# Kernel optimization log

Measured on AMD Instinct MI355X. Metric: run time of the kernel, lower is better.

## Reference

```python
import jax, jax.numpy as jnp
import numpy as np

NUM_GRAPHS = 8
NEG_SLOPE = 0.2  # PyG GATConv default negative_slope


def gat_dense(x, W, att_src, att_dst, W_edge, att_edge, bias, agg, mask):
    """Dense-masked equivalent of PyG GATConv(edge_dim=1, add_self_loops=True,
    fill_value='mean'). mask[i,j]=True means edge src=i -> dst=j."""
    N = x.shape[0]
    H, C = att_src.shape
    h = (x @ W).reshape(N, H, C)                      # [N,H,C]
    a_s = jnp.einsum('nhc,hc->nh', h, att_src)        # alpha_src per node
    a_d = jnp.einsum('nhc,hc->nh', h, att_dst)        # alpha_dst per node
    eye = jnp.eye(N, dtype=bool)
    mask_od = mask & ~eye                             # remove_self_loops
    ev = jnp.where(mask_od, agg, 0.0)                 # edge_attr (scalar per edge)
    cnt = mask_od.sum(axis=0)                         # in-degree per dst
    mean_e = jnp.where(cnt > 0, ev.sum(axis=0) / jnp.maximum(cnt, 1), 0.0)
    ev = ev + jnp.eye(N, dtype=agg.dtype) * mean_e    # add self-loops, fill='mean' per dst
    full = mask_od | eye
    # lin_edge is Linear(1, H*C, bias=False): per-head edge score is
    # e_ij * sum_c W_edge[h,c]*att_edge[h,c]
    we = (W_edge.reshape(H, C) * att_edge).sum(-1)    # [H]
    logits = jax.nn.leaky_relu(a_s[:, None, :] + a_d[None, :, :] + ev[:, :, None] * we[None, None, :], NEG_SLOPE)  # [src,dst,H]
    logits = jnp.where(full[:, :, None], logits, -jnp.inf)
    alpha = jax.nn.softmax(logits, axis=0)            # segment softmax over sources per dst
    out = jnp.einsum('sdh,shc->dhc', alpha, h).reshape(N, H * C) + bias
    return out


def setup_inputs() -> dict:
    key = jax.random.key(0)
    ks = jax.random.split(key, 20)
    N, IN, HID, H, OUT = 2048, 128, 64, 4, 10
    s = 0.05
    rn = lambda k, shp, sc=s: (jax.random.normal(k, shp, dtype=jnp.float32) * sc)
    return {
        'x': jax.random.normal(ks[0], (N, IN), dtype=jnp.float32),
        'attn_tensor': jax.random.normal(ks[1], (12, N, N), dtype=jnp.float32),
        'batch_idx': jnp.sort(jax.random.randint(ks[2], (N,), 0, NUM_GRAPHS)),
        # Conv2d(12,1,1) -> 1x1 conv == weighted sum over the 12 maps
        'w_agg': rn(ks[3], (12,), 0.2),
        'b_agg': jnp.zeros((), dtype=jnp.float32),
        # GAT layer 1: in=128 -> heads=4, out=64, concat
        'W1': rn(ks[4], (IN, H * HID)),
        'att_src1': rn(ks[5], (H, HID)),
        'att_dst1': rn(ks[6], (H, HID)),
        'We1': rn(ks[7], (1, H * HID)),
        'att_e1': rn(ks[8], (H, HID)),
        'bias1': jnp.zeros((H * HID,), dtype=jnp.float32),
        # GAT layer 2: in=256 -> heads=1, out=64
        'W2': rn(ks[9], (H * HID, HID)),
        'att_src2': rn(ks[10], (1, HID)),
        'att_dst2': rn(ks[11], (1, HID)),
        'We2': rn(ks[12], (1, HID)),
        'att_e2': rn(ks[13], (1, HID)),
        'bias2': jnp.zeros((HID,), dtype=jnp.float32),
        # final Linear(hidden, out)
        'W_lin': rn(ks[14], (HID, OUT)),
        'b_lin': jnp.zeros((OUT,), dtype=jnp.float32),
    }


def reference(x, attn_tensor, batch_idx, w_agg, b_agg, W1, att_src1, att_dst1,
              We1, att_e1, bias1, W2, att_src2, att_dst2, We2, att_e2, bias2,
              W_lin, b_lin):
    # 1x1 conv over the 12 attention maps -> [N,N]
    agg = jnp.einsum('k,kij->ij', w_agg, attn_tensor) + b_agg
    mask = agg > 0.0  # threshold
    h1 = jax.nn.elu(gat_dense(x, W1, att_src1, att_dst1, We1, att_e1, bias1, agg, mask))
    h2 = jax.nn.elu(gat_dense(h1, W2, att_src2, att_dst2, We2, att_e2, bias2, agg, mask))
    # global mean pool over graphs
    ones = jnp.ones((x.shape[0],), dtype=h2.dtype)
    cnt = jax.ops.segment_sum(ones, batch_idx, num_segments=NUM_GRAPHS)
    g = jax.ops.segment_sum(h2, batch_idx, num_segments=NUM_GRAPHS) / jnp.maximum(cnt, 1.0)[:, None]
    out = g @ W_lin + b_lin
    # edge_attr = agg[mask]; returned densely (masked) to keep static shapes
    edge_attr = jnp.where(mask, agg, 0.0)
    return out, edge_attr
```

## Files before the change

kernel.cpp:

```cpp
#include <hip/hip_runtime.h>

#define N 2048
#define NG 8

__device__ __forceinline__ float lrelu(float x) { return x > 0.f ? x : 0.2f * x; }

__global__ __launch_bounds__(256) void aggK(const float* __restrict__ attn,
                                            const float* __restrict__ w_agg,
                                            const float* __restrict__ b_agg,
                                            float* __restrict__ edge_out,
                                            float* __restrict__ aggT,
                                            float* __restrict__ colSum,
                                            float* __restrict__ colCnt) {
  __shared__ float tile[32][33];
  __shared__ float wsh[12];
  __shared__ float cs[32];
  __shared__ float cc[32];
  int tx = threadIdx.x, ty = threadIdx.y;
  int tid = ty * 32 + tx;
  if (tid < 12) wsh[tid] = w_agg[tid];
  if (tid < 32) { cs[tid] = 0.f; cc[tid] = 0.f; }
  __syncthreads();
  int i0 = blockIdx.y * 32, j0 = blockIdx.x * 32;
  int j = j0 + tx;
  float bb = b_agg[0];
#pragma unroll
  for (int r = 0; r < 4; ++r) {
    int li = ty + 8 * r;
    int i = i0 + li;
    const float* p = attn + (size_t)i * N + j;
    float v = bb;
#pragma unroll
    for (int k = 0; k < 12; ++k) v += wsh[k] * p[(size_t)k * N * N];
    float e = v > 0.f ? v : 0.f;
    edge_out[(size_t)i * N + j] = e;
    tile[li][tx] = e;
    if (e > 0.f && i != j) { atomicAdd(&cs[tx], e); atomicAdd(&cc[tx], 1.f); }
  }
  __syncthreads();
#pragma unroll
  for (int r = 0; r < 4; ++r) {
    int lj = ty + 8 * r;
    aggT[(size_t)(j0 + lj) * N + i0 + tx] = tile[tx][lj];
  }
  if (tid < 32) {
    atomicAdd(&colSum[j0 + tid], cs[tid]);
    atomicAdd(&colCnt[j0 + tid], cc[tid]);
  }
}

__global__ __launch_bounds__(256) void h1K(const float* __restrict__ x, const float* __restrict__ W1,
                                           const float* __restrict__ att_src1, const float* __restrict__ att_dst1,
                                           const float* __restrict__ We1, const float* __restrict__ att_e1,
                                           const float* __restrict__ We2, const float* __restrict__ att_e2,
                                           float* __restrict__ h1, float* __restrict__ a_s1, float* __restrict__ a_d1,
                                           float* __restrict__ we) {
  __shared__ float xr[4][128];
  int tid = threadIdx.x;
  int n0 = blockIdx.x * 4;
  if (blockIdx.x == 0) {
    float v1 = We1[tid] * att_e1[tid];
#pragma unroll
    for (int off = 32; off > 0; off >>= 1) v1 += __shfl_down(v1, off);
    int lane = tid & 63, wid = tid >> 6;
    if (lane == 0) we[wid] = v1;
    float v2 = (tid < 64) ? We2[tid] * att_e2[tid] : 0.f;
#pragma unroll
    for (int off = 32; off > 0; off >>= 1) v2 += __shfl_down(v2, off);
    if (tid == 0) we[4] = v2;
  }
  for (int t = tid; t < 512; t += 256) xr[t >> 7][t & 127] = x[n0 * 128 + t];
  __syncthreads();
  float acc[4] = {0.f, 0.f, 0.f, 0.f};
  for (int k = 0; k < 128; ++k) {
    float wv = W1[k * 256 + tid];
#pragma unroll
    for (int r = 0; r < 4; ++r) acc[r] += xr[r][k] * wv;
  }
  float asw = att_src1[tid], adw = att_dst1[tid];
  int lane = tid & 63, head = tid >> 6;
#pragma unroll
  for (int r = 0; r < 4; ++r) {
    h1[(size_t)(n0 + r) * 256 + tid] = acc[r];
    float ps = acc[r] * asw, pd = acc[r] * adw;
#pragma unroll
    for (int off = 32; off > 0; off >>= 1) { ps += __shfl_down(ps, off); pd += __shfl_down(pd, off); }
    if (lane == 0) { a_s1[(n0 + r) * 4 + head] = ps; a_d1[(n0 + r) * 4 + head] = pd; }
  }
}

__global__ __launch_bounds__(256) void pv1K(const float* __restrict__ aggT, const float* __restrict__ h1,
                                            const float* __restrict__ a_s1, const float* __restrict__ a_d1,
                                            const float* __restrict__ colSum, const float* __restrict__ colCnt,
                                            const float* __restrict__ we,
                                            float* __restrict__ partials, float* __restrict__ z1) {
  __shared__ float hT[16][260];
  __shared__ float pL[16][260];
  int tid = threadIdx.x;
  int d0 = blockIdx.x * 64;
  int sBeg = blockIdx.y * 128;
  float w0 = we[0], w1 = we[1], w2 = we[2], w3 = we[3];
  int ssp = tid & 15, dq = tid >> 4;
  float4 ad4[4];
  float me_[4];
#pragma unroll
  for (int q = 0; q < 4; ++q) {
    int d = d0 + dq * 4 + q;
    ad4[q] = *(const float4*)(a_d1 + d * 4);
    float c = colCnt[d];
    me_[q] = c > 0.f ? colSum[d] / c : 0.f;
  }
  float zac[4][4];
#pragma unroll
  for (int q = 0; q < 4; ++q)
#pragma unroll
    for (int h = 0; h < 4; ++h) zac[q][h] = 0.f;
  int dg = tid & 7;
  int cb = (tid >> 3) * 8;
  int hh = tid >> 6;
  float acc[8][8];
#pragma unroll
  for (int i = 0; i < 8; ++i)
#pragma unroll
    for (int j = 0; j < 8; ++j) acc[i][j] = 0.f;

  int c4 = (tid & 63) * 4;
  int rb = (tid >> 6) * 4;

#pragma unroll 1
  for (int s0 = sBeg; s0 < sBeg + 128; s0 += 16) {
#pragma unroll
    for (int p4 = 0; p4 < 4; ++p4) {
      int r = rb + p4;
      *(float4*)(&hT[r][c4]) = *(const float4*)(h1 + (size_t)(s0 + r) * 256 + c4);
    }
    {
      int s = s0 + ssp;
      float4 as4 = *(const float4*)(a_s1 + s * 4);
      float pq[4][4];
#pragma unroll
      for (int q = 0; q < 4; ++q) {
        int d = d0 + dq * 4 + q;
        float av = aggT[(size_t)d * N + s];
        float ev; bool inc;
        if (s == d) { ev = me_[q]; inc = true; } else { ev = av; inc = av > 0.f; }
        float p0 = inc ? __expf(lrelu(as4.x + ad4[q].x + ev * w0)) : 0.f;
        float p1 = inc ? __expf(lrelu(as4.y + ad4[q].y + ev * w1)) : 0.f;
        float p2 = inc ? __expf(lrelu(as4.z + ad4[q].z + ev * w2)) : 0.f;
        float p3 = inc ? __expf(lrelu(as4.w + ad4[q].w + ev * w3)) : 0.f;
        pq[0][q] = p0; pq[1][q] = p1; pq[2][q] = p2; pq[3][q] = p3;
        zac[q][0] += p0; zac[q][1] += p1; zac[q][2] += p2; zac[q][3] += p3;
      }
#pragma unroll
      for (int h = 0; h < 4; ++h)
        *(float4*)(&pL[ssp][h * 64 + dq * 4]) = make_float4(pq[h][0], pq[h][1], pq[h][2], pq[h][3]);
    }
    __syncthreads();
#pragma unroll
    for (int ss = 0; ss < 16; ++ss) {
      float4 pA = *(const float4*)(&pL[ss][hh * 64 + dg * 8]);
      float4 pB = *(const float4*)(&pL[ss][hh * 64 + dg * 8 + 4]);
      float4 hA = *(const float4*)(&hT[ss][cb]);
      float4 hB = *(const float4*)(&hT[ss][cb + 4]);
      float pv[8] = {pA.x, pA.y, pA.z, pA.w, pB.x, pB.y, pB.z, pB.w};
      float hv[8] = {hA.x, hA.y, hA.z, hA.w, hB.x, hB.y, hB.z, hB.w};
#pragma unroll
      for (int di = 0; di < 8; ++di)
#pragma unroll
        for (int ci = 0; ci < 8; ++ci) acc[di][ci] += pv[di] * hv[ci];
    }
    __syncthreads();
  }
  float* outp = partials + (size_t)blockIdx.y * ((size_t)N * 256);
#pragma unroll
  for (int di = 0; di < 8; ++di) {
    size_t rowo = (size_t)(d0 + dg * 8 + di) * 256 + cb;
    *(float4*)(outp + rowo) = make_float4(acc[di][0], acc[di][1], acc[di][2], acc[di][3]);
    *(float4*)(outp + rowo + 4) = make_float4(acc[di][4], acc[di][5], acc[di][6], acc[di][7]);
  }
#pragma unroll
  for (int q = 0; q < 4; ++q)
#pragma unroll
    for (int h = 0; h < 4; ++h) {
      float v = zac[q][h];
      v += __shfl_down(v, 8); v += __shfl_down(v, 4);
      v += __shfl_down(v, 2); v += __shfl_down(v, 1);
      if (ssp == 0) atomicAdd(&z1[(d0 + dq * 4 + q) * 4 + h], v);
    }
}

__global__ __launch_bounds__(256) void h2K(const float* __restrict__ partials, const float* __restrict__ z1,
                                           const float* __restrict__ bias1,
                                           const float* __restrict__ W2,
                                           const float* __restrict__ att_src2, const float* __restrict__ att_dst2,
                                           float* __restrict__ hh2, float* __restrict__ a_s2, float* __restrict__ a_d2) {
  __shared__ float hr[4][256];
  int tid = threadIdx.x;
  int n0 = blockIdx.x * 4;
  for (int e = tid; e < 1024; e += 256) {
    int node = e >> 8, c = e & 255;
    size_t base = (size_t)(n0 + node) * 256 + c;
    float sAcc = 0.f;
#pragma unroll
    for (int q = 0; q < 16; ++q) sAcc += partials[(size_t)q * N * 256 + base];
    float a = sAcc / z1[(n0 + node) * 4 + (c >> 6)] + bias1[c];
    hr[node][c] = a > 0.f ? a : __expf(a) - 1.f;
  }
  __syncthreads();
  int c = tid & 63, nl = tid >> 6;
  float acc = 0.f;
  for (int k = 0; k < 256; ++k) acc += hr[nl][k] * W2[k * 64 + c];
  hh2[(size_t)(n0 + nl) * 64 + c] = acc;
  float ps = acc * att_src2[c], pd = acc * att_dst2[c];
#pragma unroll
  for (int off = 32; off > 0; off >>= 1) { ps += __shfl_down(ps, off); pd += __shfl_down(pd, off); }
  if (c == 0) { a_s2[n0 + nl] = ps; a_d2[n0 + nl] = pd; }
}

__global__ __launch_bounds__(256) void pv2K(const float* __restrict__ aggT, const float* __restrict__ hh2,
                                            const float* __restrict__ a_s2, const float* __restrict__ a_d2,
                                            const float* __restrict__ colSum, const float* __restrict__ colCnt,
                                            const float* __restrict__ we,
                                            float* __restrict__ partials, float* __restrict__ z2) {
  __shared__ float hT[16][68];
  __shared__ float pL[16][132];
  int tid = threadIdx.x;
  int d0 = blockIdx.x * 128;
  int sBeg = blockIdx.y * 64;
  float wE = we[4];
  int ssp = tid & 15, dq = tid >> 4;
  float adv[8], me_[8];
#pragma unroll
  for (int q = 0; q < 8; ++q) {
    int d = d0 + dq * 8 + q;
    adv[q] = a_d2[d];
    float c = colCnt[d];
    me_[q] = c > 0.f ? colSum[d] / c : 0.f;
  }
  float zac[8];
#pragma unroll
  for (int q = 0; q < 8; ++q) zac[q] = 0.f;
  int dg = tid & 15;
  int cg = tid >> 4;
  float acc[8][4];
#pragma unroll
  for (int i = 0; i < 8; ++i)
#pragma unroll
    for (int j = 0; j < 4; ++j) acc[i][j] = 0.f;

  int stR = tid >> 4, stC = (tid & 15) * 4;

#pragma unroll 1
  for (int s0 = sBeg; s0 < sBeg + 64; s0 += 16) {
    *(float4*)(&hT[stR][stC]) = *(const float4*)(hh2 + (size_t)(s0 + stR) * 64 + stC);
    {
      int s = s0 + ssp;
      float asv = a_s2[s];
      float pq[8];
#pragma unroll
      for (int q = 0; q < 8; ++q) {
        int d = d0 + dq * 8 + q;
        float av = aggT[(size_t)d * N + s];
        float ev; bool inc;
        if (s == d) { ev = me_[q]; inc = true; } else { ev = av; inc = av > 0.f; }
        float p = inc ? __expf(lrelu(asv + adv[q] + ev * wE)) : 0.f;
        pq[q] = p;
        zac[q] += p;
      }
      *(float4*)(&pL[ssp][dq * 8])     = make_float4(pq[0], pq[1], pq[2], pq[3]);
      *(float4*)(&pL[ssp][dq * 8 + 4]) = make_float4(pq[4], pq[5], pq[6], pq[7]);
    }
    __syncthreads();
#pragma unroll
    for (int ss = 0; ss < 16; ++ss) {
      float4 pA = *(const float4*)(&pL[ss][dg * 8]);
      float4 pB = *(const float4*)(&pL[ss][dg * 8 + 4]);
      float4 hA = *(const float4*)(&hT[ss][cg * 4]);
      float pv[8] = {pA.x, pA.y, pA.z, pA.w, pB.x, pB.y, pB.z, pB.w};
      float hv[4] = {hA.x, hA.y, hA.z, hA.w};
#pragma unroll
      for (int di = 0; di < 8; ++di)
#pragma unroll
        for (int ci = 0; ci < 4; ++ci) acc[di][ci] += pv[di] * hv[ci];
    }
    __syncthreads();
  }
  float* outp = partials + (size_t)blockIdx.y * ((size_t)N * 64);
#pragma unroll
  for (int di = 0; di < 8; ++di) {
    size_t rowo = (size_t)(d0 + dg * 8 + di) * 64 + cg * 4;
    *(float4*)(outp + rowo) = make_float4(acc[di][0], acc[di][1], acc[di][2], acc[di][3]);
  }
#pragma unroll
  for (int q = 0; q < 8; ++q) {
    float v = zac[q];
    v += __shfl_down(v, 8); v += __shfl_down(v, 4);
    v += __shfl_down(v, 2); v += __shfl_down(v, 1);
    if (ssp == 0) atomicAdd(&z2[d0 + dq * 8 + q], v);
  }
}

__global__ __launch_bounds__(256) void fin2K(const float* __restrict__ partials, const float* __restrict__ z2,
                                             const float* __restrict__ bias2, float* __restrict__ h2post) {
  int i = blockIdx.x * 256 + threadIdx.x;
  int d = i >> 6, c = i & 63;
  float s = 0.f;
#pragma unroll
  for (int q = 0; q < 32; ++q) s += partials[(size_t)q * N * 64 + i];
  float a = s / z2[d] + bias2[c];
  h2post[i] = a > 0.f ? a : __expf(a) - 1.f;
}

__global__ __launch_bounds__(256) void poolK(const float* __restrict__ h2post, const int* __restrict__ bidx,
                                             const float* __restrict__ W_lin, const float* __restrict__ b_lin,
                                             float* __restrict__ out) {
  __shared__ float red[4][64];
  __shared__ float cntA[4];
  __shared__ float gsh[64];
  int tid = threadIdx.x;
  int b = blockIdx.x;
  int c = tid & 63, g = tid >> 6;
  float s = 0.f, cnt = 0.f;
  for (int n = g; n < N; n += 4) {
    if (bidx[n] == b) {
      s += h2post[(size_t)n * 64 + c];
      cnt += 1.f;
    }
  }
  red[g][c] = s;
  if (c == 0) cntA[g] = cnt;
  __syncthreads();
  if (g == 0) {
    float tot = red[0][c] + red[1][c] + red[2][c] + red[3][c];
    float ct = cntA[0] + cntA[1] + cntA[2] + cntA[3];
    gsh[c] = tot / fmaxf(ct, 1.f);
  }
  __syncthreads();
  if (tid < 10) {
    float o = b_lin[tid];
    for (int k = 0; k < 64; ++k) o += gsh[k] * W_lin[k * 10 + tid];
    out[b * 10 + tid] = o;
  }
}

extern "C" void kernel_launch(void* const* d_in, const int* in_sizes, int n_in,
                              void* d_out, int out_size, void* d_ws, size_t ws_size,
                              hipStream_t stream) {
  const float* x        = (const float*)d_in[0];
  const float* attn     = (const float*)d_in[1];
  const int*   bidx     = (const int*)d_in[2];
  const float* w_agg    = (const float*)d_in[3];
  const float* b_agg    = (const float*)d_in[4];
  const float* W1       = (const float*)d_in[5];
  const float* att_src1 = (const float*)d_in[6];
  const float* att_dst1 = (const float*)d_in[7];
  const float* We1      = (const float*)d_in[8];
  const float* att_e1   = (const float*)d_in[9];
  const float* bias1    = (const float*)d_in[10];
  const float* W2       = (const float*)d_in[11];
  const float* att_src2 = (const float*)d_in[12];
  const float* att_dst2 = (const float*)d_in[13];
  const float* We2      = (const float*)d_in[14];
  const float* att_e2   = (const float*)d_in[15];
  const float* bias2    = (const float*)d_in[16];
  const float* W_lin    = (const float*)d_in[17];
  const float* b_lin    = (const float*)d_in[18];

  float* out = (float*)d_out;
  float* edge_out = out + 80;

  float* w = (float*)d_ws;
  size_t o = 0;
  float* aggT   = w + o; o += (size_t)N * N;
  float* zb     = w + o; o += 7 * N;
  float* wev    = w + o; o += 8;
  float* h1     = w + o; o += (size_t)N * 256;
  float* a_s1   = w + o; o += (size_t)N * 4;
  float* a_d1   = w + o; o += (size_t)N * 4;
  float* hh2    = w + o; o += (size_t)N * 64;
  float* a_s2   = w + o; o += N;
  float* a_d2   = w + o; o += N;
  float* partials = w + o; o += (size_t)16 * N * 256;

  float* colSum = zb;
  float* colCnt = zb + N;
  float* z1     = zb + 2 * N;
  float* z2     = zb + 6 * N;
  float* h2post = hh2;

  hipMemsetAsync(zb, 0, 7 * N * sizeof(float), stream);
  aggK<<<dim3(64, 64), dim3(32, 8), 0, stream>>>(attn, w_agg, b_agg, edge_out, aggT, colSum, colCnt);
  h1K<<<512, 256, 0, stream>>>(x, W1, att_src1, att_dst1, We1, att_e1, We2, att_e2, h1, a_s1, a_d1, wev);
  pv1K<<<dim3(32, 16), 256, 0, stream>>>(aggT, h1, a_s1, a_d1, colSum, colCnt, wev, partials, z1);
  h2K<<<512, 256, 0, stream>>>(partials, z1, bias1, W2, att_src2, att_dst2, hh2, a_s2, a_d2);
  pv2K<<<dim3(16, 32), 256, 0, stream>>>(aggT, hh2, a_s2, a_d2, colSum, colCnt, wev, partials, z2);
  fin2K<<<512, 256, 0, stream>>>(partials, z2, bias2, h2post);
  poolK<<<NG, 256, 0, stream>>>(h2post, bidx, W_lin, b_lin, out);
}
```

Before: 549.6 us.

## Drop transposed agg copy, fuse agg with h1 and fin2 with pooling

The separate transposed aggT matrix is removed. Both attention-value kernels now read the row-major edge_out output directly, using float4 loads along the destination dimension, which avoids writing and re-reading a 16 MB buffer. The aggregation and h1 projection kernels are merged into one launch split by block index, so they can run concurrently. fin2 and pooling are merged using atomics and a last-block ticket that computes the final linear layer. This saves launches and memory traffic, at the cost of global atomics and a nondeterministic summation order in pooling.

```diff
diff --git a/kernel.cpp b/kernel.cpp
--- a/kernel.cpp
+++ b/kernel.cpp
@@ -5,91 +5,85 @@
 
 __device__ __forceinline__ float lrelu(float x) { return x > 0.f ? x : 0.2f * x; }
 
-__global__ __launch_bounds__(256) void aggK(const float* __restrict__ attn,
-                                            const float* __restrict__ w_agg,
-                                            const float* __restrict__ b_agg,
-                                            float* __restrict__ edge_out,
-                                            float* __restrict__ aggT,
-                                            float* __restrict__ colSum,
-                                            float* __restrict__ colCnt) {
-  __shared__ float tile[32][33];
-  __shared__ float wsh[12];
-  __shared__ float cs[32];
-  __shared__ float cc[32];
-  int tx = threadIdx.x, ty = threadIdx.y;
-  int tid = ty * 32 + tx;
-  if (tid < 12) wsh[tid] = w_agg[tid];
-  if (tid < 32) { cs[tid] = 0.f; cc[tid] = 0.f; }
-  __syncthreads();
-  int i0 = blockIdx.y * 32, j0 = blockIdx.x * 32;
-  int j = j0 + tx;
-  float bb = b_agg[0];
-#pragma unroll
-  for (int r = 0; r < 4; ++r) {
-    int li = ty + 8 * r;
-    int i = i0 + li;
-    const float* p = attn + (size_t)i * N + j;
-    float v = bb;
-#pragma unroll
-    for (int k = 0; k < 12; ++k) v += wsh[k] * p[(size_t)k * N * N];
-    float e = v > 0.f ? v : 0.f;
-    edge_out[(size_t)i * N + j] = e;
-    tile[li][tx] = e;
-    if (e > 0.f && i != j) { atomicAdd(&cs[tx], e); atomicAdd(&cc[tx], 1.f); }
-  }
-  __syncthreads();
-#pragma unroll
-  for (int r = 0; r < 4; ++r) {
-    int lj = ty + 8 * r;
-    aggT[(size_t)(j0 + lj) * N + i0 + tx] = tile[tx][lj];
-  }
-  if (tid < 32) {
-    atomicAdd(&colSum[j0 + tid], cs[tid]);
-    atomicAdd(&colCnt[j0 + tid], cc[tid]);
-  }
-}
-
-__global__ __launch_bounds__(256) void h1K(const float* __restrict__ x, const float* __restrict__ W1,
-                                           const float* __restrict__ att_src1, const float* __restrict__ att_dst1,
-                                           const float* __restrict__ We1, const float* __restrict__ att_e1,
-                                           const float* __restrict__ We2, const float* __restrict__ att_e2,
-                                           float* __restrict__ h1, float* __restrict__ a_s1, float* __restrict__ a_d1,
-                                           float* __restrict__ we) {
-  __shared__ float xr[4][128];
-  int tid = threadIdx.x;
-  int n0 = blockIdx.x * 4;
-  if (blockIdx.x == 0) {
-    float v1 = We1[tid] * att_e1[tid];
-#pragma unroll
-    for (int off = 32; off > 0; off >>= 1) v1 += __shfl_down(v1, off);
-    int lane = tid & 63, wid = tid >> 6;
-    if (lane == 0) we[wid] = v1;
-    float v2 = (tid < 64) ? We2[tid] * att_e2[tid] : 0.f;
-#pragma unroll
-    for (int off = 32; off > 0; off >>= 1) v2 += __shfl_down(v2, off);
-    if (tid == 0) we[4] = v2;
-  }
-  for (int t = tid; t < 512; t += 256) xr[t >> 7][t & 127] = x[n0 * 128 + t];
-  __syncthreads();
-  float acc[4] = {0.f, 0.f, 0.f, 0.f};
-  for (int k = 0; k < 128; ++k) {
-    float wv = W1[k * 256 + tid];
-#pragma unroll
-    for (int r = 0; r < 4; ++r) acc[r] += xr[r][k] * wv;
-  }
-  float asw = att_src1[tid], adw = att_dst1[tid];
-  int lane = tid & 63, head = tid >> 6;
-#pragma unroll
-  for (int r = 0; r < 4; ++r) {
-    h1[(size_t)(n0 + r) * 256 + tid] = acc[r];
-    float ps = acc[r] * asw, pd = acc[r] * adw;
-#pragma unroll
-    for (int off = 32; off > 0; off >>= 1) { ps += __shfl_down(ps, off); pd += __shfl_down(pd, off); }
-    if (lane == 0) { a_s1[(n0 + r) * 4 + head] = ps; a_d1[(n0 + r) * 4 + head] = pd; }
-  }
-}
-
-__global__ __launch_bounds__(256) void pv1K(const float* __restrict__ aggT, const float* __restrict__ h1,
+__global__ __launch_bounds__(256) void aggh1K(const float* __restrict__ attn,
+                                              const float* __restrict__ w_agg,
+                                              const float* __restrict__ b_agg,
+                                              const float* __restrict__ x,
+                                              const float* __restrict__ W1,
+                                              const float* __restrict__ att_src1,
+                                              const float* __restrict__ att_dst1,
+                                              const float* __restrict__ We1, const float* __restrict__ att_e1,
+                                              const float* __restrict__ We2, const float* __restrict__ att_e2,
+                                              float* __restrict__ edge_out,
+                                              float* __restrict__ colSum, float* __restrict__ colCnt,
+                                              float* __restrict__ h1, float* __restrict__ a_s1, float* __restrict__ a_d1,
+                                              float* __restrict__ we) {
+  __shared__ float smem[512];
+  int tid = threadIdx.x;
+  if (blockIdx.x < 512) {
+    float* xr = smem;
+    int n0 = blockIdx.x * 4;
+    if (blockIdx.x == 0) {
+      float v1 = We1[tid] * att_e1[tid];
+#pragma unroll
+      for (int off = 32; off > 0; off >>= 1) v1 += __shfl_down(v1, off);
+      int lane = tid & 63, wid = tid >> 6;
+      if (lane == 0) we[wid] = v1;
+      float v2 = (tid < 64) ? We2[tid] * att_e2[tid] : 0.f;
+#pragma unroll
+      for (int off = 32; off > 0; off >>= 1) v2 += __shfl_down(v2, off);
+      if (tid == 0) we[4] = v2;
+    }
+    for (int t = tid; t < 512; t += 256) xr[t] = x[n0 * 128 + t];
+    __syncthreads();
+    float acc[4] = {0.f, 0.f, 0.f, 0.f};
+    for (int k = 0; k < 128; ++k) {
+      float wv = W1[k * 256 + tid];
+#pragma unroll
+      for (int r = 0; r < 4; ++r) acc[r] += xr[r * 128 + k] * wv;
+    }
+    float asw = att_src1[tid], adw = att_dst1[tid];
+    int lane = tid & 63, head = tid >> 6;
+#pragma unroll
+    for (int r = 0; r < 4; ++r) {
+      h1[(size_t)(n0 + r) * 256 + tid] = acc[r];
+      float ps = acc[r] * asw, pd = acc[r] * adw;
+#pragma unroll
+      for (int off = 32; off > 0; off >>= 1) { ps += __shfl_down(ps, off); pd += __shfl_down(pd, off); }
+      if (lane == 0) { a_s1[(n0 + r) * 4 + head] = ps; a_d1[(n0 + r) * 4 + head] = pd; }
+    }
+  } else {
+    float* wsh = smem;
+    float* cs = smem + 32;
+    float* cc = smem + 64;
+    int bidA = blockIdx.x - 512;
+    int tx = tid & 31, ty = tid >> 5;
+    if (tid < 12) wsh[tid] = w_agg[tid];
+    if (tid < 32) { cs[tid] = 0.f; cc[tid] = 0.f; }
+    __syncthreads();
+    int i0 = (bidA >> 6) * 32, j0 = (bidA & 63) * 32;
+    int j = j0 + tx;
+    float bb = b_agg[0];
+#pragma unroll
+    for (int r = 0; r < 4; ++r) {
+      int i = i0 + ty + 8 * r;
+      const float* p = attn + (size_t)i * N + j;
+      float v = bb;
+#pragma unroll
+      for (int k = 0; k < 12; ++k) v += wsh[k] * p[(size_t)k * N * N];
+      float e = v > 0.f ? v : 0.f;
+      edge_out[(size_t)i * N + j] = e;
+      if (e > 0.f && i != j) { atomicAdd(&cs[tx], e); atomicAdd(&cc[tx], 1.f); }
+    }
+    __syncthreads();
+    if (tid < 32) {
+      atomicAdd(&colSum[j0 + tid], cs[tid]);
+      atomicAdd(&colCnt[j0 + tid], cc[tid]);
+    }
+  }
+}
+
+__global__ __launch_bounds__(256) void pv1K(const float* __restrict__ edge, const float* __restrict__ h1,
                                             const float* __restrict__ a_s1, const float* __restrict__ a_d1,
                                             const float* __restrict__ colSum, const float* __restrict__ colCnt,
                                             const float* __restrict__ we,
@@ -137,11 +131,13 @@
     {
       int s = s0 + ssp;
       float4 as4 = *(const float4*)(a_s1 + s * 4);
+      float4 av4 = *(const float4*)(edge + (size_t)s * N + d0 + dq * 4);
+      float ev_[4] = {av4.x, av4.y, av4.z, av4.w};
       float pq[4][4];
 #pragma unroll
       for (int q = 0; q < 4; ++q) {
         int d = d0 + dq * 4 + q;
-        float av = aggT[(size_t)d * N + s];
+        float av = ev_[q];
         float ev; bool inc;
         if (s == d) { ev = me_[q]; inc = true; } else { ev = av; inc = av > 0.f; }
         float p0 = inc ? __expf(lrelu(as4.x + ad4[q].x + ev * w0)) : 0.f;
@@ -217,7 +213,7 @@
   if (c == 0) { a_s2[n0 + nl] = ps; a_d2[n0 + nl] = pd; }
 }
 
-__global__ __launch_bounds__(256) void pv2K(const float* __restrict__ aggT, const float* __restrict__ hh2,
+__global__ __launch_bounds__(256) void pv2K(const float* __restrict__ edge, const float* __restrict__ hh2,
                                             const float* __restrict__ a_s2, const float* __restrict__ a_d2,
                                             const float* __restrict__ colSum, const float* __restrict__ colCnt,
                                             const float* __restrict__ we,
@@ -256,11 +252,14 @@
     {
       int s = s0 + ssp;
       float asv = a_s2[s];
+      float4 eA = *(const float4*)(edge + (size_t)s * N + d0 + dq * 8);
+      float4 eB = *(const float4*)(edge + (size_t)s * N + d0 + dq * 8 + 4);
+      float ev_[8] = {eA.x, eA.y, eA.z, eA.w, eB.x, eB.y, eB.z, eB.w};
       float pq[8];
 #pragma unroll
       for (int q = 0; q < 8; ++q) {
         int d = d0 + dq * 8 + q;
-        float av = aggT[(size_t)d * N + s];
+        float av = ev_[q];
         float ev; bool inc;
         if (s == d) { ev = me_[q]; inc = true; } else { ev = av; inc = av > 0.f; }
         float p = inc ? __expf(lrelu(asv + adv[q] + ev * wE)) : 0.f;
@@ -300,46 +299,46 @@
   }
 }
 
-__global__ __launch_bounds__(256) void fin2K(const float* __restrict__ partials, const float* __restrict__ z2,
-                                             const float* __restrict__ bias2, float* __restrict__ h2post) {
-  int i = blockIdx.x * 256 + threadIdx.x;
+__global__ __launch_bounds__(256) void fin2poolK(const float* __restrict__ partials, const float* __restrict__ z2,
+                                                 const float* __restrict__ bias2, const int* __restrict__ bidx,
+                                                 const float* __restrict__ W_lin, const float* __restrict__ b_lin,
+                                                 float* __restrict__ gsum, float* __restrict__ gcnt,
+                                                 int* __restrict__ ticket, float* __restrict__ out) {
+  int tid = threadIdx.x;
+  int i = blockIdx.x * 256 + tid;
   int d = i >> 6, c = i & 63;
   float s = 0.f;
 #pragma unroll
   for (int q = 0; q < 32; ++q) s += partials[(size_t)q * N * 64 + i];
   float a = s / z2[d] + bias2[c];
-  h2post[i] = a > 0.f ? a : __expf(a) - 1.f;
-}
-
-__global__ __launch_bounds__(256) void poolK(const float* __restrict__ h2post, const int* __restrict__ bidx,
-                                             const float* __restrict__ W_lin, const float* __restrict__ b_lin,
-                                             float* __restrict__ out) {
-  __shared__ float red[4][64];
-  __shared__ float cntA[4];
-  __shared__ float gsh[64];
-  int tid = threadIdx.x;
-  int b = blockIdx.x;
-  int c = tid & 63, g = tid >> 6;
-  float s = 0.f, cnt = 0.f;
-  for (int n = g; n < N; n += 4) {
-    if (bidx[n] == b) {
-      s += h2post[(size_t)n * 64 + c];
-      cnt += 1.f;
-    }
-  }
-  red[g][c] = s;
-  if (c == 0) cntA[g] = cnt;
+  float v = a > 0.f ? a : __expf(a) - 1.f;
+  int g = bidx[d];
+  atomicAdd(&gsum[g * 64 + c], v);
+  if (c == 0) atomicAdd(&gcnt[g], 1.f);
+  __threadfence();
   __syncthreads();
-  if (g == 0) {
-    float tot = red[0][c] + red[1][c] + red[2][c] + red[3][c];
-    float ct = cntA[0] + cntA[1] + cntA[2] + cntA[3];
-    gsh[c] = tot / fmaxf(ct, 1.f);
+  __shared__ int lastSh;
+  if (tid == 0) {
+    int t = atomicAdd(ticket, 1);
+    lastSh = (t == (int)gridDim.x - 1) ? 1 : 0;
   }
   __syncthreads();
-  if (tid < 10) {
-    float o = b_lin[tid];
-    for (int k = 0; k < 64; ++k) o += gsh[k] * W_lin[k * 10 + tid];
-    out[b * 10 + tid] = o;
+  if (lastSh) {
+    __shared__ float gm[NG][64];
+    __shared__ float cnt_[NG];
+    if (tid < NG) cnt_[tid] = atomicAdd(&gcnt[tid], 0.f);
+    __syncthreads();
+    for (int e = tid; e < NG * 64; e += 256) {
+      float sv = atomicAdd(&gsum[e], 0.f);
+      gm[e >> 6][e & 63] = sv / fmaxf(cnt_[e >> 6], 1.f);
+    }
+    __syncthreads();
+    if (tid < NG * 10) {
+      int b = tid / 10, o = tid % 10;
+      float accv = b_lin[o];
+      for (int k = 0; k < 64; ++k) accv += gm[b][k] * W_lin[k * 10 + o];
+      out[b * 10 + o] = accv;
+    }
   }
 }
 
@@ -371,29 +370,30 @@
 
   float* w = (float*)d_ws;
   size_t o = 0;
-  float* aggT   = w + o; o += (size_t)N * N;
-  float* zb     = w + o; o += 7 * N;
-  float* wev    = w + o; o += 8;
-  float* h1     = w + o; o += (size_t)N * 256;
-  float* a_s1   = w + o; o += (size_t)N * 4;
-  float* a_d1   = w + o; o += (size_t)N * 4;
-  float* hh2    = w + o; o += (size_t)N * 64;
-  float* a_s2   = w + o; o += N;
-  float* a_d2   = w + o; o += N;
+  float* zb   = w + o; o += 7 * N + 1024;
+  float* wev  = w + o; o += 8;
+  float* h1   = w + o; o += (size_t)N * 256;
+  float* a_s1 = w + o; o += (size_t)N * 4;
+  float* a_d1 = w + o; o += (size_t)N * 4;
+  float* hh2  = w + o; o += (size_t)N * 64;
+  float* a_s2 = w + o; o += N;
+  float* a_d2 = w + o; o += N;
   float* partials = w + o; o += (size_t)16 * N * 256;
 
   float* colSum = zb;
   float* colCnt = zb + N;
   float* z1     = zb + 2 * N;
   float* z2     = zb + 6 * N;
-  float* h2post = hh2;
-
-  hipMemsetAsync(zb, 0, 7 * N * sizeof(float), stream);
-  aggK<<<dim3(64, 64), dim3(32, 8), 0, stream>>>(attn, w_agg, b_agg, edge_out, aggT, colSum, colCnt);
-  h1K<<<512, 256, 0, stream>>>(x, W1, att_src1, att_dst1, We1, att_e1, We2, att_e2, h1, a_s1, a_d1, wev);
-  pv1K<<<dim3(32, 16), 256, 0, stream>>>(aggT, h1, a_s1, a_d1, colSum, colCnt, wev, partials, z1);
+  float* gsum   = zb + 7 * N;
+  float* gcnt   = zb + 7 * N + 512;
+  int*   ticket = (int*)(zb + 7 * N + 520);
+
+  hipMemsetAsync(zb, 0, (7 * N + 1024) * sizeof(float), stream);
+  aggh1K<<<4608, 256, 0, stream>>>(attn, w_agg, b_agg, x, W1, att_src1, att_dst1,
+                                   We1, att_e1, We2, att_e2,
+                                   edge_out, colSum, colCnt, h1, a_s1, a_d1, wev);
+  pv1K<<<dim3(32, 16), 256, 0, stream>>>(edge_out, h1, a_s1, a_d1, colSum, colCnt, wev, partials, z1);
   h2K<<<512, 256, 0, stream>>>(partials, z1, bias1, W2, att_src2, att_dst2, hh2, a_s2, a_d2);
-  pv2K<<<dim3(16, 32), 256, 0, stream>>>(aggT, hh2, a_s2, a_d2, colSum, colCnt, wev, partials, z2);
-  fin2K<<<512, 256, 0, stream>>>(partials, z2, bias2, h2post);
-  poolK<<<NG, 256, 0, stream>>>(h2post, bidx, W_lin, b_lin, out);
-}
+  pv2K<<<dim3(16, 32), 256, 0, stream>>>(edge_out, hh2, a_s2, a_d2, colSum, colCnt, wev, partials, z2);
+  fin2poolK<<<512, 256, 0, stream>>>(partials, z2, bias2, bidx, W_lin, b_lin, gsum, gcnt, ticket, out);
+}
```

After: 481.6 us. -12.4%, faster.
